# Performance work log

Measured on AMD Instinct MI355X. Metric: run time of the kernel, lower is better.

The kernel has to match this reference:

```python
import jax, jax.numpy as jnp
import numpy as np

TEMP = 0.5
EPS = 1e-12  # matches torch F.normalize default eps


def _l2_normalize(x):
    n = jnp.sqrt(jnp.sum(x * x, axis=1, keepdims=True))
    return x / jnp.maximum(n, EPS)


def setup_inputs() -> dict:
    key = jax.random.key(0)
    k1, k2 = jax.random.split(key)
    B, D = 4096, 256
    return {
        "x_i": jax.random.normal(k1, (B, D), dtype=jnp.float32),
        "x_j": jax.random.normal(k2, (B, D), dtype=jnp.float32),
    }


def reference(x_i, x_j):
    B = x_i.shape[0]
    z = jnp.concatenate([_l2_normalize(x_i), _l2_normalize(x_j)], axis=0)  # [2B, D]
    # cosine similarity of normalized vectors == plain matmul
    sim = z @ z.T  # [2B, 2B]
    pos = jnp.concatenate([jnp.diagonal(sim, B), jnp.diagonal(sim, -B)], axis=0)  # [2B]
    neg_mask = 1.0 - jnp.eye(2 * B, dtype=sim.dtype)
    denom = jnp.sum(neg_mask * jnp.exp(sim / TEMP), axis=1)  # [2B]
    # -log(exp(pos/T) / denom) = -pos/T + log(denom)
    loss = jnp.sum(-(pos / TEMP) + jnp.log(denom)) / (2 * B)
    return loss
```

## Files before the change

### kernel.cpp

```cpp
#include <hip/hip_runtime.h>
#include <hip/hip_bf16.h>

#define B_ROWS 4096
#define NROWS  8192
#define D      256
#define TT     264
#define NBLK2  1024

typedef __attribute__((ext_vector_type(8))) short bf16x8;
typedef __attribute__((ext_vector_type(4))) float floatx4;

__global__ __launch_bounds__(256) void norm_pos_kernel(
    const float* __restrict__ xi, const float* __restrict__ xj,
    short* __restrict__ z, float* __restrict__ pos,
    float* __restrict__ selfdot, float* __restrict__ rowsum,
    float* __restrict__ out, unsigned int* __restrict__ counter) {
    int gt = blockIdx.x * 256 + threadIdx.x;
    if (gt < NROWS) rowsum[gt] = 0.f;
    if (gt == 0) { out[0] = 0.f; counter[0] = 0u; }

    int p    = blockIdx.x * 4 + (threadIdx.x >> 6);
    int lane = threadIdx.x & 63;
    float4 v1 = ((const float4*)(xi + (size_t)p * D))[lane];
    float4 v2 = ((const float4*)(xj + (size_t)p * D))[lane];
    float ss1 = v1.x * v1.x + v1.y * v1.y + v1.z * v1.z + v1.w * v1.w;
    float ss2 = v2.x * v2.x + v2.y * v2.y + v2.z * v2.z + v2.w * v2.w;
#pragma unroll
    for (int off = 32; off > 0; off >>= 1) {
        ss1 += __shfl_xor(ss1, off);
        ss2 += __shfl_xor(ss2, off);
    }
    float sc1 = 1.0f / fmaxf(sqrtf(ss1), 1e-12f);
    float sc2 = 1.0f / fmaxf(sqrtf(ss2), 1e-12f);

    union { __hip_bfloat16 h[4]; short4 s4; } u1, u2;
    u1.h[0] = __float2bfloat16(v1.x * sc1); u1.h[1] = __float2bfloat16(v1.y * sc1);
    u1.h[2] = __float2bfloat16(v1.z * sc1); u1.h[3] = __float2bfloat16(v1.w * sc1);
    u2.h[0] = __float2bfloat16(v2.x * sc2); u2.h[1] = __float2bfloat16(v2.y * sc2);
    u2.h[2] = __float2bfloat16(v2.z * sc2); u2.h[3] = __float2bfloat16(v2.w * sc2);
    ((short4*)(z + (size_t)p * D))[lane]            = u1.s4;
    ((short4*)(z + (size_t)(p + B_ROWS) * D))[lane] = u2.s4;

    float sd1 = 0.f, sd2 = 0.f, dp = 0.f;
#pragma unroll
    for (int j = 0; j < 4; j++) {
        float a = __bfloat162float(u1.h[j]);
        float b = __bfloat162float(u2.h[j]);
        sd1 += a * a; sd2 += b * b; dp += a * b;
    }
#pragma unroll
    for (int off = 32; off > 0; off >>= 1) {
        sd1 += __shfl_xor(sd1, off);
        sd2 += __shfl_xor(sd2, off);
        dp  += __shfl_xor(dp,  off);
    }
    if (lane == 0) {
        pos[p] = dp; pos[p + B_ROWS] = dp;
        selfdot[p] = sd1; selfdot[p + B_ROWS] = sd2;
    }
}

__global__ __launch_bounds__(256, 4) void sim_rowsum_kernel(
    const short* __restrict__ z, float* __restrict__ rowsum,
    const float* __restrict__ pos, const float* __restrict__ selfdot,
    unsigned int* __restrict__ counter, float* __restrict__ out) {
    __shared__ __align__(16) short Bbuf[2][8192];
    __shared__ unsigned int done_s;
    __shared__ float sdata[4];

    const int tid  = threadIdx.x;
    const int lane = tid & 63;
    const int w    = tid >> 6;
    const int lm   = lane & 15;
    const int lg   = lane >> 4;
    const int fxor = lm & 7;

    const int bid = blockIdx.x;
    const int s   = bid >> 6;
    const int q   = (bid >> 1) & 31;
    const int h   = bid & 1;
    const int L0  = 256 - 8 * s;
    const int cb  = (q * TT) >> 5;
    const int ce  = ((q + 1) * TT) >> 5;

    bf16x8 a[8][2];
    floatx4 acc[2][2];
    float rsacc[2][4];

#pragma unroll
    for (int mi = 0; mi < 2; mi++)
#pragma unroll
        for (int r = 0; r < 4; r++) rsacc[mi][r] = 0.f;

    auto decode = [&](int c, int& panel, int& colbase, bool& mirror) {
        int cloc;
        if (c < L0) { panel = s;      cloc = c; }
        else        { panel = 31 - s; cloc = c - L0; }
        colbase = panel * 256 + cloc * 32;
        mirror  = (cloc >= 8);
    };

    auto decodeCol = [&](int c) {
        int cloc, panel;
        if (c < L0) { panel = s;      cloc = c; }
        else        { panel = 31 - s; cloc = c - L0; }
        return panel * 256 + cloc * 32;
    };

    auto loadA = [&](int panel) {
#pragma unroll
        for (int kk = 0; kk < 8; kk++)
#pragma unroll
            for (int mi = 0; mi < 2; mi++)
                a[kk][mi] = *(const bf16x8*)(
                    z + (size_t)(panel * 256 + h * 128 + w * 32 + mi * 16 + lm) * D +
                    kk * 32 + lg * 8);
    };

    auto flushRs = [&](int panel) {
#pragma unroll
        for (int mi = 0; mi < 2; mi++)
#pragma unroll
            for (int r = 0; r < 4; r++) {
                float v = rsacc[mi][r];
                v += __shfl_xor(v, 1); v += __shfl_xor(v, 2);
                v += __shfl_xor(v, 4); v += __shfl_xor(v, 8);
                if (lm == 0)
                    atomicAdd(&rowsum[panel * 256 + h * 128 + w * 32 + mi * 16 +
                                      lg * 4 + r], v);
                rsacc[mi][r] = 0.f;
            }
    };

    auto stage = [&](int buf, int colbase) {
#pragma unroll
        for (int j = 0; j < 4; j++) {
            int col = w * 8 + j * 2 + (lane >> 5);
            int c16 = (lane & 31) ^ (col & 7);
            const short* src = z + (size_t)(colbase + col) * D + c16 * 8;
            __builtin_amdgcn_global_load_lds(
                (const __attribute__((address_space(1))) unsigned int*)src,
                (__attribute__((address_space(3))) unsigned int*)
                    &Bbuf[buf][(w * 4 + j) * 512],
                16, 0, 0);
        }
    };

    int panel, colbase; bool mirror;
    decode(cb, panel, colbase, mirror);
    int curpanel = panel;
    stage(0, colbase);
    loadA(panel);
    __syncthreads();

    for (int c = cb; c < ce; c++) {
        const int buf = (c - cb) & 1;
        decode(c, panel, colbase, mirror);

        if (c + 1 < ce)
            stage(buf ^ 1, decodeCol(c + 1));

        if (panel != curpanel) {
            flushRs(curpanel);
            loadA(panel);
            curpanel = panel;
        }

#pragma unroll
        for (int mi = 0; mi < 2; mi++)
#pragma unroll
            for (int ni = 0; ni < 2; ni++)
                acc[mi][ni] = (floatx4){0.f, 0.f, 0.f, 0.f};

#pragma unroll
        for (int kk = 0; kk < 8; kk++) {
            bf16x8 b0 = *(const bf16x8*)(
                &Bbuf[buf][((lm) * 32 + ((kk * 4 + lg) ^ fxor)) * 8]);
            bf16x8 b1 = *(const bf16x8*)(
                &Bbuf[buf][((16 + lm) * 32 + ((kk * 4 + lg) ^ fxor)) * 8]);
            acc[0][0] = __builtin_amdgcn_mfma_f32_16x16x32_bf16(
                a[kk][0], b0, acc[0][0], 0, 0, 0);
            acc[1][0] = __builtin_amdgcn_mfma_f32_16x16x32_bf16(
                a[kk][1], b0, acc[1][0], 0, 0, 0);
            acc[0][1] = __builtin_amdgcn_mfma_f32_16x16x32_bf16(
                a[kk][0], b1, acc[0][1], 0, 0, 0);
            acc[1][1] = __builtin_amdgcn_mfma_f32_16x16x32_bf16(
                a[kk][1], b1, acc[1][1], 0, 0, 0);
        }

        float cs0 = 0.f, cs1 = 0.f;
#pragma unroll
        for (int mi = 0; mi < 2; mi++)
#pragma unroll
            for (int r = 0; r < 4; r++) {
                float e0 = __expf(2.0f * acc[mi][0][r]);
                float e1 = __expf(2.0f * acc[mi][1][r]);
                rsacc[mi][r] += e0 + e1;
                cs0 += e0; cs1 += e1;
            }
        if (mirror) {
            cs0 += __shfl_xor(cs0, 16); cs0 += __shfl_xor(cs0, 32);
            cs1 += __shfl_xor(cs1, 16); cs1 += __shfl_xor(cs1, 32);
            if (lane < 16) {
                atomicAdd(&rowsum[colbase + lane],      cs0);
                atomicAdd(&rowsum[colbase + 16 + lane], cs1);
            }
        }

        __syncthreads();
    }
    flushRs(curpanel);

    __syncthreads();
    if (tid == 0) {
        __threadfence();
        done_s = atomicAdd(counter, 1u);
    }
    __syncthreads();
    if (done_s == (unsigned int)(NBLK2 - 1)) {
        __threadfence();
        float acc_l = 0.f;
#pragma unroll 4
        for (int r = tid; r < NROWS; r += 256) {
            float rsv = __hip_atomic_load(&rowsum[r], __ATOMIC_RELAXED,
                                          __HIP_MEMORY_SCOPE_AGENT);
            float denom = rsv - __expf(2.0f * selfdot[r]);
            acc_l += -2.0f * pos[r] + logf(denom);
        }
#pragma unroll
        for (int off = 32; off > 0; off >>= 1) acc_l += __shfl_xor(acc_l, off);
        if (lane == 0) sdata[w] = acc_l;
        __syncthreads();
        if (tid == 0)
            out[0] = (sdata[0] + sdata[1] + sdata[2] + sdata[3]) / (float)NROWS;
    }
}

extern "C" void kernel_launch(void* const* d_in, const int* in_sizes, int n_in,
                              void* d_out, int out_size, void* d_ws, size_t ws_size,
                              hipStream_t stream) {
    const float* xi = (const float*)d_in[0];
    const float* xj = (const float*)d_in[1];
    float* out      = (float*)d_out;

    char* ws        = (char*)d_ws;
    short* z        = (short*)ws;
    float* rowsum   = (float*)(ws + (size_t)NROWS * D * 2);
    float* pos      = rowsum + NROWS;
    float* selfdot  = pos + NROWS;
    unsigned int* counter = (unsigned int*)(selfdot + NROWS);

    norm_pos_kernel<<<B_ROWS / 4, 256, 0, stream>>>(xi, xj, z, pos, selfdot,
                                                    rowsum, out, counter);
    sim_rowsum_kernel<<<NBLK2, 256, 0, stream>>>(z, rowsum, pos, selfdot,
                                                 counter, out);
}
```

Before: 113.7 us.

## Double per-block row tile and batch mirror column sums in LDS

Each block now covers all 256 rows of a panel instead of 128, with each wave holding 64 rows (4 MFMA row tiles). This halves the block count and doubles reuse of every staged B column tile. Mirror column partial sums are first accumulated in a small LDS array and flushed to global atomics once at the end, cutting global atomic traffic. In exchange, register pressure rises (A fragments double) and occupancy drops to 2 blocks per CU, with fewer blocks available to balance load.

```diff
diff --git a/kernel.cpp b/kernel.cpp
--- a/kernel.cpp
+++ b/kernel.cpp
@@ -5,7 +5,8 @@
 #define NROWS  8192
 #define D      256
 #define TT     264
-#define NBLK2  1024
+#define NBLK2  512
+#define MAXT   9
 
 typedef __attribute__((ext_vector_type(8))) short bf16x8;
 typedef __attribute__((ext_vector_type(4))) float floatx4;
@@ -60,11 +61,12 @@
     }
 }
 
-__global__ __launch_bounds__(256, 4) void sim_rowsum_kernel(
+__global__ __launch_bounds__(256, 2) void sim_rowsum_kernel(
     const short* __restrict__ z, float* __restrict__ rowsum,
     const float* __restrict__ pos, const float* __restrict__ selfdot,
     unsigned int* __restrict__ counter, float* __restrict__ out) {
     __shared__ __align__(16) short Bbuf[2][8192];
+    __shared__ float mirror_lds[MAXT][32];
     __shared__ unsigned int done_s;
     __shared__ float sdata[4];
 
@@ -75,20 +77,18 @@
     const int lg   = lane >> 4;
     const int fxor = lm & 7;
 
-    const int bid = blockIdx.x;
-    const int s   = bid >> 6;
-    const int q   = (bid >> 1) & 31;
-    const int h   = bid & 1;
+    const int s   = blockIdx.x >> 5;
+    const int q   = blockIdx.x & 31;
     const int L0  = 256 - 8 * s;
     const int cb  = (q * TT) >> 5;
     const int ce  = ((q + 1) * TT) >> 5;
 
-    bf16x8 a[8][2];
-    floatx4 acc[2][2];
-    float rsacc[2][4];
-
-#pragma unroll
-    for (int mi = 0; mi < 2; mi++)
+    bf16x8 a[8][4];
+    floatx4 acc[4][2];
+    float rsacc[4][4];
+
+#pragma unroll
+    for (int mi = 0; mi < 4; mi++)
 #pragma unroll
         for (int r = 0; r < 4; r++) rsacc[mi][r] = 0.f;
 
@@ -111,23 +111,22 @@
 #pragma unroll
         for (int kk = 0; kk < 8; kk++)
 #pragma unroll
-            for (int mi = 0; mi < 2; mi++)
+            for (int mi = 0; mi < 4; mi++)
                 a[kk][mi] = *(const bf16x8*)(
-                    z + (size_t)(panel * 256 + h * 128 + w * 32 + mi * 16 + lm) * D +
+                    z + (size_t)(panel * 256 + w * 64 + mi * 16 + lm) * D +
                     kk * 32 + lg * 8);
     };
 
     auto flushRs = [&](int panel) {
 #pragma unroll
-        for (int mi = 0; mi < 2; mi++)
+        for (int mi = 0; mi < 4; mi++)
 #pragma unroll
             for (int r = 0; r < 4; r++) {
                 float v = rsacc[mi][r];
                 v += __shfl_xor(v, 1); v += __shfl_xor(v, 2);
                 v += __shfl_xor(v, 4); v += __shfl_xor(v, 8);
                 if (lm == 0)
-                    atomicAdd(&rowsum[panel * 256 + h * 128 + w * 32 + mi * 16 +
-                                      lg * 4 + r], v);
+                    atomicAdd(&rowsum[panel * 256 + w * 64 + mi * 16 + lg * 4 + r], v);
                 rsacc[mi][r] = 0.f;
             }
     };
@@ -146,6 +145,9 @@
         }
     };
 
+    for (int e = tid; e < MAXT * 32; e += 256)
+        ((float*)mirror_lds)[e] = 0.f;
+
     int panel, colbase; bool mirror;
     decode(cb, panel, colbase, mirror);
     int curpanel = panel;
@@ -167,7 +169,7 @@
         }
 
 #pragma unroll
-        for (int mi = 0; mi < 2; mi++)
+        for (int mi = 0; mi < 4; mi++)
 #pragma unroll
             for (int ni = 0; ni < 2; ni++)
                 acc[mi][ni] = (floatx4){0.f, 0.f, 0.f, 0.f};
@@ -178,19 +180,19 @@
                 &Bbuf[buf][((lm) * 32 + ((kk * 4 + lg) ^ fxor)) * 8]);
             bf16x8 b1 = *(const bf16x8*)(
                 &Bbuf[buf][((16 + lm) * 32 + ((kk * 4 + lg) ^ fxor)) * 8]);
-            acc[0][0] = __builtin_amdgcn_mfma_f32_16x16x32_bf16(
-                a[kk][0], b0, acc[0][0], 0, 0, 0);
-            acc[1][0] = __builtin_amdgcn_mfma_f32_16x16x32_bf16(
-                a[kk][1], b0, acc[1][0], 0, 0, 0);
-            acc[0][1] = __builtin_amdgcn_mfma_f32_16x16x32_bf16(
-                a[kk][0], b1, acc[0][1], 0, 0, 0);
-            acc[1][1] = __builtin_amdgcn_mfma_f32_16x16x32_bf16(
-                a[kk][1], b1, acc[1][1], 0, 0, 0);
+#pragma unroll
+            for (int mi = 0; mi < 4; mi++)
+                acc[mi][0] = __builtin_amdgcn_mfma_f32_16x16x32_bf16(
+                    a[kk][mi], b0, acc[mi][0], 0, 0, 0);
+#pragma unroll
+            for (int mi = 0; mi < 4; mi++)
+                acc[mi][1] = __builtin_amdgcn_mfma_f32_16x16x32_bf16(
+                    a[kk][mi], b1, acc[mi][1], 0, 0, 0);
         }
 
         float cs0 = 0.f, cs1 = 0.f;
 #pragma unroll
-        for (int mi = 0; mi < 2; mi++)
+        for (int mi = 0; mi < 4; mi++)
 #pragma unroll
             for (int r = 0; r < 4; r++) {
                 float e0 = __expf(2.0f * acc[mi][0][r]);
@@ -202,14 +204,25 @@
             cs0 += __shfl_xor(cs0, 16); cs0 += __shfl_xor(cs0, 32);
             cs1 += __shfl_xor(cs1, 16); cs1 += __shfl_xor(cs1, 32);
             if (lane < 16) {
-                atomicAdd(&rowsum[colbase + lane],      cs0);
-                atomicAdd(&rowsum[colbase + 16 + lane], cs1);
+                atomicAdd(&mirror_lds[c - cb][lane],      cs0);
+                atomicAdd(&mirror_lds[c - cb][16 + lane], cs1);
             }
         }
 
         __syncthreads();
     }
     flushRs(curpanel);
+
+    __syncthreads();
+    {
+        const int nt = ce - cb;
+        for (int e = tid; e < nt * 32; e += 256) {
+            int t = e >> 5, col = e & 31;
+            int p2, cbase2; bool m2;
+            decode(cb + t, p2, cbase2, m2);
+            if (m2) atomicAdd(&rowsum[cbase2 + col], mirror_lds[t][col]);
+        }
+    }
 
     __syncthreads();
     if (tid == 0) {
```

Measured after the change: 103.7 us. 8.8% less time.
